# Performance work log

Hardware: AMD Instinct MI355X
Metric: run time of the kernel (lower is better)

The kernel has to match this reference:

```python
import jax, jax.numpy as jnp
import numpy as np

ALPHA = 0.2  # LeakyReLU negative slope
NEG_INF = -1e12


def setup_inputs() -> dict:
    key = jax.random.key(0)
    k1, k2, k3, k4 = jax.random.split(key, 4)
    B, N, F_in, F_out = 8, 4096, 128, 64
    inp = jax.random.normal(k1, (B, N, F_in), dtype=jnp.float32)
    adj = jax.random.randint(k2, (B, N, N), 0, 2, dtype=jnp.int32)
    # xavier-uniform-ish init for W, a
    W = jax.random.normal(k3, (F_in, F_out), dtype=jnp.float32) * (2.0 / (F_in + F_out)) ** 0.5
    a = jax.random.normal(k4, (2 * F_out, 1), dtype=jnp.float32) * (2.0 / (2 * F_out + 1)) ** 0.5
    return {"inp": inp, "adj": adj, "W": W, "a": a}


def reference(inp, adj, W, a):
    # inp: [B,N,F_in], adj: [B,N,N] int, W: [F_in,F_out], a: [2*F_out,1]
    F_out = W.shape[1]
    h = jnp.einsum('bnf,fo->bno', inp, W)          # [B,N,F_out]
    a1 = a[:F_out, 0]                              # [F_out]
    a2 = a[F_out:, 0]                              # [F_out]
    # e[b,i,j] = leakyrelu(h_i . a1 + h_j . a2)  (== concat([h_i,h_j]) @ a)
    s1 = h @ a1                                    # [B,N]
    s2 = h @ a2                                    # [B,N]
    e = s1[:, :, None] + s2[:, None, :]            # [B,N,N]
    e = jnp.where(e > 0, e, ALPHA * e)             # LeakyReLU
    att = jnp.where(adj > 0, e, NEG_INF)
    att = jax.nn.softmax(att, axis=-1)             # [B,N,N]
    # dropout p=0.0 -> identity
    h_prime = jnp.einsum('bij,bjo->bio', att, h)   # [B,N,F_out]
    return jax.nn.elu(h_prime)
```

## Files before the change

### kernel.cpp

```cpp
#include <hip/hip_runtime.h>
#include <hip/hip_bf16.h>
#include <cstdint>

typedef __attribute__((ext_vector_type(8))) short short8;
typedef __attribute__((ext_vector_type(4))) float floatx4;

#define LEAKY_ALPHA 0.2f

__device__ __forceinline__ unsigned short f2bf_rne(float f) {
    unsigned u = __float_as_uint(f);
    unsigned r = u + 0x7FFFu + ((u >> 16) & 1u);
    return (unsigned short)(r >> 16);
}

__global__ __launch_bounds__(256) void k_pack(const int* __restrict__ adj,
                                              unsigned* __restrict__ mask) {
    const size_t t = (size_t)blockIdx.x * 256 + threadIdx.x;
    const int* p = adj + t * 32;
    unsigned m = 0;
    #pragma unroll
    for (int k = 0; k < 8; ++k) {
        const int4 v = *(const int4*)(p + k * 4);
        m |= (v.x > 0 ? 1u : 0u) << (k * 4 + 0);
        m |= (v.y > 0 ? 1u : 0u) << (k * 4 + 1);
        m |= (v.z > 0 ? 1u : 0u) << (k * 4 + 2);
        m |= (v.w > 0 ? 1u : 0u) << (k * 4 + 3);
    }
    mask[t] = m;
}

__global__ __launch_bounds__(256) void k_h(const float* __restrict__ inp,
                                           const float* __restrict__ W,
                                           const float* __restrict__ a,
                                           unsigned short* __restrict__ hT,
                                           float* __restrict__ s1,
                                           float* __restrict__ s2) {
    __shared__ float hs[64][65];
    const int tid  = threadIdx.x;
    const int wv   = tid >> 6;
    const int lane = tid & 63;
    const int blk  = blockIdx.x;
    const int b     = blk >> 6;
    const int ibase = (blk & 63) * 64;

    const float a1 = a[lane];
    const float a2 = a[64 + lane];

    for (int rr = 0; rr < 16; ++rr) {
        const int rloc = wv * 16 + rr;
        const int row  = ibase + rloc;
        const float* ip = inp + ((size_t)(b * 4096 + row)) * 128;
        float acc = 0.f;
        #pragma unroll
        for (int f = 0; f < 128; f += 4) {
            float4 v = *(const float4*)(ip + f);
            acc += v.x * W[(f + 0) * 64 + lane];
            acc += v.y * W[(f + 1) * 64 + lane];
            acc += v.z * W[(f + 2) * 64 + lane];
            acc += v.w * W[(f + 3) * 64 + lane];
        }
        hs[rloc][lane] = acc;
        float r1 = acc * a1;
        float r2 = acc * a2;
        #pragma unroll
        for (int off = 32; off > 0; off >>= 1) {
            r1 += __shfl_xor(r1, off);
            r2 += __shfl_xor(r2, off);
        }
        if (lane == 0) {
            s1[b * 4096 + row] = r1;
            s2[b * 4096 + row] = r2;
        }
    }
    __syncthreads();

    const int n  = tid >> 2;
    const int iq = tid & 3;
    unsigned pk[8];
    #pragma unroll
    for (int s = 0; s < 16; s += 2) {
        unsigned lo = f2bf_rne(hs[iq * 16 + s    ][n]);
        unsigned hi = f2bf_rne(hs[iq * 16 + s + 1][n]);
        pk[s >> 1] = lo | (hi << 16);
    }
    unsigned short* dst = hT + ((size_t)(b * 64 + n)) * 4096 + ibase + iq * 16;
    *(int4*)(dst)     = *(int4*)&pk[0];
    *(int4*)(dst + 8) = *(int4*)&pk[4];
}

__global__ __launch_bounds__(256, 4) void k_attn(const unsigned* __restrict__ mask,
                                                 const unsigned short* __restrict__ hT,
                                                 const float* __restrict__ s1g,
                                                 const float* __restrict__ s2g,
                                                 float* __restrict__ out) {
    __shared__ float s2s[4096];
    __shared__ float accbuf[2][64][17];
    __shared__ float lbuf[2][64];

    const int tid   = threadIdx.x;
    const int b     = blockIdx.x >> 7;
    const int rtile = blockIdx.x & 127;

    {
        const float* src = s2g + b * 4096;
        #pragma unroll
        for (int t = 0; t < 4; ++t) {
            int idx = tid * 16 + t * 4;
            *(float4*)&s2s[idx] = *(const float4*)(src + idx);
        }
    }
    __syncthreads();

    const int wv    = tid >> 6;
    const int lane  = tid & 63;
    const int jhalf = wv >> 1;
    const int m     = lane & 15;
    const int kh    = lane >> 4;
    const int rbase = rtile * 32 + (wv & 1) * 16;
    const int row   = rbase + m;

    const float s1v = s1g[b * 4096 + row];
    const int jb0 = jhalf * 2048 + kh * 8;
    const unsigned* mrow = mask + ((size_t)(b * 4096 + row)) * 128 + jhalf * 64;
    const unsigned short* hrow0 = hT + ((size_t)(b * 64 +  0 + m)) * 4096 + jb0;
    const unsigned short* hrow1 = hT + ((size_t)(b * 64 + 16 + m)) * 4096 + jb0;
    const unsigned short* hrow2 = hT + ((size_t)(b * 64 + 32 + m)) * 4096 + jb0;
    const unsigned short* hrow3 = hT + ((size_t)(b * 64 + 48 + m)) * 4096 + jb0;

    floatx4 acc0 = (floatx4){0.f,0.f,0.f,0.f};
    floatx4 acc1 = (floatx4){0.f,0.f,0.f,0.f};
    floatx4 acc2 = (floatx4){0.f,0.f,0.f,0.f};
    floatx4 acc3 = (floatx4){0.f,0.f,0.f,0.f};
    float lsum = 0.f;

    unsigned rm_0, rm_1;
    short8 rb0_0, rb1_0, rb2_0, rb3_0, rb0_1, rb1_1, rb2_1, rb3_1;

    rm_0  = mrow[0];
    rb0_0 = *(const short8*)(hrow0);       rb1_0 = *(const short8*)(hrow1);
    rb2_0 = *(const short8*)(hrow2);       rb3_0 = *(const short8*)(hrow3);
    rm_1  = mrow[1];
    rb0_1 = *(const short8*)(hrow0 + 32);  rb1_1 = *(const short8*)(hrow1 + 32);
    rb2_1 = *(const short8*)(hrow2 + 32);  rb3_1 = *(const short8*)(hrow3 + 32);

#define GAT_STEP(SL, STEPIDX)                                                  \
    do {                                                                       \
        const unsigned cmw = rm_##SL;                                          \
        const short8 cb0 = rb0_##SL, cb1 = rb1_##SL;                           \
        const short8 cb2 = rb2_##SL, cb3 = rb3_##SL;                           \
        const int pstep = ((STEPIDX) + 2) & 63;         \
        const int poff = pstep * 32;                                           \
        rm_##SL  = mrow[pstep];                                                \
        rb0_##SL = *(const short8*)(hrow0 + poff);                             \
        rb1_##SL = *(const short8*)(hrow1 + poff);                             \
        rb2_##SL = *(const short8*)(hrow2 + poff);                             \
        rb3_##SL = *(const short8*)(hrow3 + poff);                             \
        const int soff = jb0 + (STEPIDX) * 32;                                 \
        const float4 csa = *(const float4*)&s2s[soff];                         \
        const float4 csb = *(const float4*)&s2s[soff + 4];                     \
        const unsigned mb = (cmw >> (kh * 8)) & 0xffu;                         \
        const float sv[8] = {csa.x, csa.y, csa.z, csa.w,                       \
                             csb.x, csb.y, csb.z, csb.w};                      \
        short8 af;                                                             \
        float psum = 0.f;                                                      \
        _Pragma("unroll")                                                      \
        for (int t = 0; t < 8; ++t) {                                          \
            float e = s1v + sv[t];                                             \
            e = fmaxf(e, LEAKY_ALPHA * e);                                     \
            float pv = ((mb >> t) & 1u) ? __expf(e) : 0.f;                     \
            psum += pv;                                                        \
            af[t] = (short)f2bf_rne(pv);                                       \
        }                                                                      \
        lsum += psum;                                                          \
        acc0 = __builtin_amdgcn_mfma_f32_16x16x32_bf16(af, cb0, acc0, 0,0,0);  \
        acc1 = __builtin_amdgcn_mfma_f32_16x16x32_bf16(af, cb1, acc1, 0,0,0);  \
        acc2 = __builtin_amdgcn_mfma_f32_16x16x32_bf16(af, cb2, acc2, 0,0,0);  \
        acc3 = __builtin_amdgcn_mfma_f32_16x16x32_bf16(af, cb3, acc3, 0,0,0);  \
    } while (0)

    #pragma unroll 1
    for (int it = 0; it < 32; ++it) {
        const int s0 = it * 2;
        GAT_STEP(0, s0);
        GAT_STEP(1, s0 + 1);
    }
#undef GAT_STEP

    lsum += __shfl_xor(lsum, 16);
    lsum += __shfl_xor(lsum, 32);

    floatx4 accs[4] = {acc0, acc1, acc2, acc3};

    if (wv >= 2) {
        #pragma unroll
        for (int f = 0; f < 4; ++f)
            #pragma unroll
            for (int r = 0; r < 4; ++r)
                accbuf[wv - 2][lane][f * 4 + r] = accs[f][r];
        lbuf[wv - 2][lane] = lsum;
    }
    __syncthreads();
    if (wv < 2) {
        const float ltot = lsum + lbuf[wv][lane];
        #pragma unroll
        for (int f = 0; f < 4; ++f) {
            #pragma unroll
            for (int r = 0; r < 4; ++r) {
                float v = accs[f][r] + accbuf[wv][lane][f * 4 + r];
                const int drow = (lane >> 4) * 4 + r;
                const float lr = __shfl(ltot, drow);
                const float hp = v / lr;
                const float o  = (hp > 0.f) ? hp : (__expf(hp) - 1.f);
                out[((size_t)(b * 4096 + rbase + drow)) * 64 + f * 16 + (lane & 15)] = o;
            }
        }
    }
}

extern "C" void kernel_launch(void* const* d_in, const int* in_sizes, int n_in,
                              void* d_out, int out_size, void* d_ws, size_t ws_size,
                              hipStream_t stream) {
    const float* inp = (const float*)d_in[0];
    const int*   adj = (const int*)d_in[1];
    const float* W   = (const float*)d_in[2];
    const float* a   = (const float*)d_in[3];
    float* out = (float*)d_out;

    unsigned short* hT = (unsigned short*)d_ws;
    float* s1 = (float*)((char*)d_ws + (size_t)8 * 64 * 4096 * 2);
    float* s2 = s1 + 8 * 4096;
    unsigned* mask = (unsigned*)(s2 + 8 * 4096);

    k_pack<<<16384, 256, 0, stream>>>(adj, mask);
    k_h<<<512, 256, 0, stream>>>(inp, W, a, hT, s1, s2);
    k_attn<<<1024, 256, 0, stream>>>(mask, hT, s1, s2, out);
}
```

Baseline: 892.4 us.

## Fuse adjacency bit-packing into attention kernel via shared-memory mask

```diff
diff --git a/kernel.cpp b/kernel.cpp
--- a/kernel.cpp
+++ b/kernel.cpp
@@ -11,22 +11,6 @@
     unsigned u = __float_as_uint(f);
     unsigned r = u + 0x7FFFu + ((u >> 16) & 1u);
     return (unsigned short)(r >> 16);
-}
-
-__global__ __launch_bounds__(256) void k_pack(const int* __restrict__ adj,
-                                              unsigned* __restrict__ mask) {
-    const size_t t = (size_t)blockIdx.x * 256 + threadIdx.x;
-    const int* p = adj + t * 32;
-    unsigned m = 0;
-    #pragma unroll
-    for (int k = 0; k < 8; ++k) {
-        const int4 v = *(const int4*)(p + k * 4);
-        m |= (v.x > 0 ? 1u : 0u) << (k * 4 + 0);
-        m |= (v.y > 0 ? 1u : 0u) << (k * 4 + 1);
-        m |= (v.z > 0 ? 1u : 0u) << (k * 4 + 2);
-        m |= (v.w > 0 ? 1u : 0u) << (k * 4 + 3);
-    }
-    mask[t] = m;
 }
 
 __global__ __launch_bounds__(256) void k_h(const float* __restrict__ inp,
@@ -88,18 +72,19 @@
     *(int4*)(dst + 8) = *(int4*)&pk[4];
 }
 
-__global__ __launch_bounds__(256, 4) void k_attn(const unsigned* __restrict__ mask,
-                                                 const unsigned short* __restrict__ hT,
-                                                 const float* __restrict__ s1g,
-                                                 const float* __restrict__ s2g,
-                                                 float* __restrict__ out) {
+__global__ __launch_bounds__(256, 4) void k_fused(const int* __restrict__ adj,
+                                                  const unsigned short* __restrict__ hT,
+                                                  const float* __restrict__ s1g,
+                                                  const float* __restrict__ s2g,
+                                                  float* __restrict__ out) {
+    __shared__ unsigned maskw[32][129];
     __shared__ float s2s[4096];
-    __shared__ float accbuf[2][64][17];
-    __shared__ float lbuf[2][64];
 
     const int tid   = threadIdx.x;
     const int b     = blockIdx.x >> 7;
     const int rtile = blockIdx.x & 127;
+    const int wv    = tid >> 6;
+    const int lane  = tid & 63;
 
     {
         const float* src = s2g + b * 4096;
@@ -109,19 +94,37 @@
             *(float4*)&s2s[idx] = *(const float4*)(src + idx);
         }
     }
-    __syncthreads();
-
-    const int wv    = tid >> 6;
-    const int lane  = tid & 63;
+
+    {
+        const int* abase = adj + ((size_t)(b * 4096 + rtile * 32)) * 4096
+                         + (size_t)wv * 32768;
+        #pragma unroll 2
+        for (int i = 0; i < 16; ++i) {
+            const int* p = abase + i * 2048 + lane * 32;
+            unsigned w = 0;
+            #pragma unroll
+            for (int k = 0; k < 8; ++k) {
+                const int4 v = *(const int4*)(p + k * 4);
+                w |= (v.x > 0 ? 1u : 0u) << (k * 4 + 0);
+                w |= (v.y > 0 ? 1u : 0u) << (k * 4 + 1);
+                w |= (v.z > 0 ? 1u : 0u) << (k * 4 + 2);
+                w |= (v.w > 0 ? 1u : 0u) << (k * 4 + 3);
+            }
+            maskw[wv * 8 + (i >> 1)][(i & 1) * 64 + lane] = w;
+        }
+    }
+    __syncthreads();
+
     const int jhalf = wv >> 1;
     const int m     = lane & 15;
     const int kh    = lane >> 4;
+    const int rl    = (wv & 1) * 16 + m;
     const int rbase = rtile * 32 + (wv & 1) * 16;
     const int row   = rbase + m;
 
     const float s1v = s1g[b * 4096 + row];
     const int jb0 = jhalf * 2048 + kh * 8;
-    const unsigned* mrow = mask + ((size_t)(b * 4096 + row)) * 128 + jhalf * 64;
+    const unsigned* mrow = &maskw[rl][jhalf * 64];
     const unsigned short* hrow0 = hT + ((size_t)(b * 64 +  0 + m)) * 4096 + jb0;
     const unsigned short* hrow1 = hT + ((size_t)(b * 64 + 16 + m)) * 4096 + jb0;
     const unsigned short* hrow2 = hT + ((size_t)(b * 64 + 32 + m)) * 4096 + jb0;
@@ -191,22 +194,26 @@
 
     floatx4 accs[4] = {acc0, acc1, acc2, acc3};
 
+    float* accb = (float*)&maskw[0][0];
+    float* lb   = accb + 2 * 64 * 17;
+
+    __syncthreads();
     if (wv >= 2) {
         #pragma unroll
         for (int f = 0; f < 4; ++f)
             #pragma unroll
             for (int r = 0; r < 4; ++r)
-                accbuf[wv - 2][lane][f * 4 + r] = accs[f][r];
-        lbuf[wv - 2][lane] = lsum;
+                accb[(wv - 2) * 64 * 17 + lane * 17 + f * 4 + r] = accs[f][r];
+        lb[(wv - 2) * 64 + lane] = lsum;
     }
     __syncthreads();
     if (wv < 2) {
-        const float ltot = lsum + lbuf[wv][lane];
+        const float ltot = lsum + lb[wv * 64 + lane];
         #pragma unroll
         for (int f = 0; f < 4; ++f) {
             #pragma unroll
             for (int r = 0; r < 4; ++r) {
-                float v = accs[f][r] + accbuf[wv][lane][f * 4 + r];
+                float v = accs[f][r] + accb[wv * 64 * 17 + lane * 17 + f * 4 + r];
                 const int drow = (lane >> 4) * 4 + r;
                 const float lr = __shfl(ltot, drow);
                 const float hp = v / lr;
@@ -229,9 +236,7 @@
     unsigned short* hT = (unsigned short*)d_ws;
     float* s1 = (float*)((char*)d_ws + (size_t)8 * 64 * 4096 * 2);
     float* s2 = s1 + 8 * 4096;
-    unsigned* mask = (unsigned*)(s2 + 8 * 4096);
-
-    k_pack<<<16384, 256, 0, stream>>>(adj, mask);
+
     k_h<<<512, 256, 0, stream>>>(inp, W, a, hT, s1, s2);
-    k_attn<<<1024, 256, 0, stream>>>(mask, hT, s1, s2, out);
-}
+    k_fused<<<1024, 256, 0, stream>>>(adj, hT, s1, s2, out);
+}
```

Measured after the change: 861.6 us. -3.5%, faster.
